# Kernel optimization log

Measured on AMD Instinct MI355X. Metric: run time of the kernel, lower is better.

Reference implementation:

```python
import jax, jax.numpy as jnp
import numpy as np

V, K, H, B = 50000, 50, 300, 512
C_WEIGHTS = 0.0005
C_TOPICS = 5e-06
BN_EPS = 1e-5


def _bn(x, g, b, m, v):
    # eval-mode BatchNorm1d with running stats
    return (x - m) * jax.lax.rsqrt(v + BN_EPS) * g + b


def setup_inputs() -> dict:
    key = jax.random.key(0)
    ks = jax.random.split(key, 16)
    s = 0.02
    inp = {
        "bows": jax.random.uniform(ks[0], (B, V), jnp.float32),
        "normalized_bows": jax.random.uniform(ks[1], (B, V), jnp.float32),
        "labels": jax.random.normal(ks[2], (B,), jnp.float32),
        # encoder q_theta: Linear(V,H) -> relu -> BN -> Linear(H,H) -> relu -> BN
        "W1": jax.random.normal(ks[3], (H, V), jnp.float32) * s,
        "b1": jnp.zeros((H,), jnp.float32),
        "W2": jax.random.normal(ks[4], (H, H), jnp.float32) * s,
        "b2": jnp.zeros((H,), jnp.float32),
        "bn1_g": jnp.ones((H,), jnp.float32),
        "bn1_b": jnp.zeros((H,), jnp.float32),
        "bn1_m": jnp.zeros((H,), jnp.float32),
        "bn1_v": jnp.ones((H,), jnp.float32),
        "bn2_g": jnp.ones((H,), jnp.float32),
        "bn2_b": jnp.zeros((H,), jnp.float32),
        "bn2_m": jnp.zeros((H,), jnp.float32),
        "bn2_v": jnp.ones((H,), jnp.float32),
        "muW": jax.random.normal(ks[5], (K, H), jnp.float32) * s,
        "mub": jnp.zeros((K,), jnp.float32),
        "lsW": jax.random.normal(ks[6], (K, H), jnp.float32) * s,
        "lsb": jnp.zeros((K,), jnp.float32),
        "logit_betas": jax.random.normal(ks[7], (V, K), jnp.float32),
        "gammas": jax.random.normal(ks[8], (V, K), jnp.float32),
        "base_rates": jax.random.normal(ks[9], (V,), jnp.float32),
        "bow_w": jax.random.normal(ks[10], (V,), jnp.float32) * s,
        "bow_b": jnp.zeros((), jnp.float32),
        "topic_w": jax.random.normal(ks[11], (K,), jnp.float32) * s,
        "topic_b": jnp.zeros((), jnp.float32),
    }
    return inp


def reference(bows, normalized_bows, labels, W1, b1, W2, b2,
              bn1_g, bn1_b, bn1_m, bn1_v, bn2_g, bn2_b, bn2_m, bn2_v,
              muW, mub, lsW, lsb, logit_betas, gammas, base_rates,
              bow_w, bow_b, topic_w, topic_b):
    # ---- encode (eval mode: reparameterize returns mu) ----
    h = _bn(jax.nn.relu(normalized_bows @ W1.T + b1), bn1_g, bn1_b, bn1_m, bn1_v)
    h = _bn(jax.nn.relu(h @ W2.T + b2), bn2_g, bn2_b, bn2_m, bn2_v)
    mu = h @ muW.T + mub                       # [B, K]
    logsigma = h @ lsW.T + lsb                 # [B, K]
    kld_theta = -0.5 * jnp.mean(jnp.sum(1.0 + logsigma - mu ** 2 - jnp.exp(logsigma), axis=-1))
    theta = jax.nn.softmax(mu, axis=-1)        # [B, K]

    # ---- decode + reconstruction loss ----
    logits = theta @ logit_betas.T + base_rates          # [B, V]
    preds = jnp.log(jax.nn.softmax(logits, axis=-1) + 1e-06)
    recon_loss = -jnp.mean(jnp.sum(preds * bows, axis=1))

    # ---- other_loss: L1 on base_rates ----
    other_loss = C_WEIGHTS * jnp.sum(jnp.abs(base_rates))

    # ---- predict_labels (hstm-all), reordered contraction: (bows @ scaled_beta) * theta
    scaled_beta = logit_betas * gammas                   # [V, K]
    het_term = jnp.sum((normalized_bows @ scaled_beta) * theta, axis=1)  # == (bows * (theta @ scaled_beta.T)).sum(1)
    expected_pred = het_term + (normalized_bows @ bow_w + bow_b) + (theta @ topic_w + topic_b)

    other_loss = other_loss + jnp.mean((expected_pred - labels) ** 2)
    other_loss = other_loss + C_TOPICS * jnp.sum(jnp.abs(gammas))
    other_loss = other_loss + C_WEIGHTS * jnp.linalg.norm(bow_w)

    return recon_loss, other_loss, kld_theta
```

## Files before the change

kernel.cpp:

```cpp
#include <hip/hip_runtime.h>
#include <hip/hip_bf16.h>
#include <math.h>


#define B_  512
#define V_  50000
#define VP  50016
#define K_  50
#define H_  300
#define KP  64
#define NW  384
#define NSTEP 1563
#define NCVT 7327
#define NSB  782

typedef __attribute__((ext_vector_type(8))) short short8;
typedef __attribute__((ext_vector_type(4))) float f32x4;

static __device__ __forceinline__ short bf16s(float f) {
  unsigned int u = __builtin_bit_cast(unsigned int, f);
  u += 0x7fffu + ((u >> 16) & 1u);
  return (short)(u >> 16);
}

static __device__ __forceinline__ unsigned int pkbf(float lo, float hi) {
  __hip_bfloat162 t = __float22bfloat162_rn(float2{lo, hi});
  unsigned int u; __builtin_memcpy(&u, &t, 4); return u;
}

static __device__ __forceinline__ short8 to_bf8(float4 a, float4 b) {
  unsigned int u[4];
  u[0] = pkbf(a.x, a.y); u[1] = pkbf(a.z, a.w);
  u[2] = pkbf(b.x, b.y); u[3] = pkbf(b.z, b.w);
  short8 r; __builtin_memcpy(&r, u, 16); return r;
}

__global__ __launch_bounds__(256) void k_prep(
    const float* __restrict__ W1,
    const float* __restrict__ beta, const float* __restrict__ gamma,
    const float* __restrict__ br,   const float* __restrict__ bw,
    short* __restrict__ Wcat, short* __restrict__ betab,
    float* __restrict__ pg, float* __restrict__ pbr, float* __restrict__ pbw2)
{
  __shared__ short sbt[64 * 52];
  __shared__ short bbt[64 * 52];
  __shared__ float redA[4];
  const int tid = threadIdx.x;

  if (blockIdx.x < NCVT) {
    const int idx = blockIdx.x * 256 + tid;
    if (idx >= 300 * (VP / 8)) return;
    const int r = idx / (VP / 8);
    const int c = (idx - r * (VP / 8)) * 8;
    short8 outv;
    if (c + 8 <= V_) {
      const float4* p = (const float4*)(W1 + (size_t)r * V_ + c);
      outv = to_bf8(p[0], p[1]);
    } else {
      outv = short8{0, 0, 0, 0, 0, 0, 0, 0};
    }
    *(short8*)(Wcat + (size_t)r * VP + c) = outv;
    return;
  }

  const int blk = blockIdx.x - NCVT;
  const int v0 = blk * 64;
  const int nvalid = (V_ - v0 < 64) ? (V_ - v0) : 64;
  const int nwrite = (VP - v0 < 64) ? (VP - v0) : 64;

  const int nf4 = (nvalid * 50) / 4;
  const float4* bsrc = (const float4*)(beta  + (size_t)v0 * 50);
  const float4* gsrc = (const float4*)(gamma + (size_t)v0 * 50);
  float gabs = 0.f;
  for (int f = tid; f < nf4; f += 256) {
    float4 bv = bsrc[f];
    float4 gv = gsrc[f];
    float be[4] = {bv.x, bv.y, bv.z, bv.w};
    float ge[4] = {gv.x, gv.y, gv.z, gv.w};
    #pragma unroll
    for (int e = 0; e < 4; ++e) {
      int idx = f * 4 + e;
      int j = idx / 50, k = idx - j * 50;
      gabs += fabsf(ge[e]);
      bbt[j * 52 + k] = bf16s(be[e]);
      sbt[j * 52 + k] = bf16s(be[e] * ge[e]);
    }
  }
  #pragma unroll
  for (int off = 1; off < 64; off <<= 1) gabs += __shfl_xor(gabs, off, 64);
  if ((tid & 63) == 0) redA[tid >> 6] = gabs;
  if (tid < 64) {
    float s1 = 0.f, s2 = 0.f;
    if (tid < nvalid) {
      s1 = fabsf(br[v0 + tid]);
      float w = bw[v0 + tid]; s2 = w * w;
    }
    #pragma unroll
    for (int off = 1; off < 64; off <<= 1) {
      s1 += __shfl_xor(s1, off, 64);
      s2 += __shfl_xor(s2, off, 64);
    }
    if (tid == 0) { pbr[blk] = s1; pbw2[blk] = s2; }
  }
  __syncthreads();
  if (tid == 0) pg[blk] = redA[0] + redA[1] + redA[2] + redA[3];

  const int j = tid & 63;
  const int q = tid >> 6;
  #pragma unroll
  for (int p = 0; p < 21; ++p) {
    const int kk = p * 4 + q;
    if (j < nwrite) {
      short val = 0;
      if (j < nvalid) {
        if (kk >= 20 && kk < 70)      val = sbt[j * 52 + (kk - 20)];
        else if (kk == 70)            val = bf16s(bw[v0 + j]);
      }
      Wcat[(size_t)(300 + kk) * VP + v0 + j] = val;
    }
  }
  if (j < nvalid) {
    __attribute__((aligned(16))) short tmp[16];
    #pragma unroll
    for (int t = 0; t < 16; ++t) {
      int k = q * 16 + t;
      tmp[t] = (k < K_) ? bbt[j * 52 + k] : (short)0;
    }
    short8* dst = (short8*)(betab + (size_t)(v0 + j) * 64 + q * 16);
    dst[0] = *(const short8*)&tmp[0];
    dst[1] = *(const short8*)&tmp[8];
  }
}

__global__ __launch_bounds__(256, 2) void k_bg(
    const float* __restrict__ A, const short* __restrict__ Wcat,
    float* __restrict__ part, int sps)
{
  const int t = blockIdx.x;
  const int s = t / 12;
  const int r = t % 12;
  const int bni = r % 3, bmi = r / 3;
  const int lane = threadIdx.x & 63, wv = threadIdx.x >> 6;
  const int l15 = lane & 15, quad = lane >> 4;
  const int m0 = bmi * 128 + (wv & 1) * 64;
  const int n0 = bni * 128 + (wv >> 1) * 64;
  int st0 = s * sps;
  int st1 = st0 + sps; if (st1 > NSTEP) st1 = NSTEP;

  const float* ap[4]; const short* bp[4];
  #pragma unroll
  for (int i = 0; i < 4; ++i) ap[i] = A + (size_t)(m0 + 16 * i + l15) * V_;
  #pragma unroll
  for (int jj = 0; jj < 4; ++jj) bp[jj] = Wcat + (size_t)(n0 + 16 * jj + l15) * VP;

  f32x4 acc[4][4];
  #pragma unroll
  for (int i = 0; i < 4; ++i)
    #pragma unroll
    for (int jj = 0; jj < 4; ++jj) acc[i][jj] = f32x4{0.f, 0.f, 0.f, 0.f};

  float4 A0[4][2], A1[4][2];
  short8 B0[4], B1[4];

  auto ld = [&](int st, float4 (&Ar)[4][2], short8 (&Br)[4]) {
    const int kk = st * 32 + quad * 8;
    if (st != 1562) {
      #pragma unroll
      for (int i = 0; i < 4; ++i) {
        const float4* p = (const float4*)(ap[i] + kk);
        Ar[i][0] = p[0]; Ar[i][1] = p[1];
      }
    } else {
      const float4 z{0.f, 0.f, 0.f, 0.f};
      #pragma unroll
      for (int i = 0; i < 4; ++i) {
        if (quad < 2) {
          const float4* p = (const float4*)(ap[i] + kk);
          Ar[i][0] = p[0]; Ar[i][1] = p[1];
        } else { Ar[i][0] = z; Ar[i][1] = z; }
      }
    }
    #pragma unroll
    for (int jj = 0; jj < 4; ++jj) Br[jj] = *(const short8*)(bp[jj] + kk);
  };
  auto comp = [&](float4 (&Ar)[4][2], short8 (&Br)[4]) {
    short8 af[4];
    #pragma unroll
    for (int i = 0; i < 4; ++i) af[i] = to_bf8(Ar[i][0], Ar[i][1]);
    #pragma unroll
    for (int i = 0; i < 4; ++i)
      #pragma unroll
      for (int jj = 0; jj < 4; ++jj)
        acc[i][jj] = __builtin_amdgcn_mfma_f32_16x16x32_bf16(af[i], Br[jj], acc[i][jj], 0, 0, 0);
  };

  if (st0 < st1) {
    ld(st0, A0, B0);
    int st = st0;
    for (; st + 2 <= st1; st += 2) {
      ld(st + 1, A1, B1);
      comp(A0, B0);
      if (st + 2 < st1) ld(st + 2, A0, B0);
      comp(A1, B1);
    }
    if (st < st1) comp(A0, B0);
  }
  float* op = part + (size_t)s * (B_ * NW);
  #pragma unroll
  for (int i = 0; i < 4; ++i)
    #pragma unroll
    for (int jj = 0; jj < 4; ++jj)
      #pragma unroll
      for (int rr = 0; rr < 4; ++rr)
        op[(size_t)(m0 + 16 * i + quad * 4 + rr) * NW + (n0 + 16 * jj + l15)] = acc[i][jj][rr];
}

__global__ __launch_bounds__(320) void k_mlp(
    const float* __restrict__ part, int S,
    const float* __restrict__ b1,
    const float* __restrict__ g1, const float* __restrict__ bb1,
    const float* __restrict__ m1, const float* __restrict__ v1,
    const float* __restrict__ W2, const float* __restrict__ b2,
    const float* __restrict__ g2, const float* __restrict__ bb2,
    const float* __restrict__ m2, const float* __restrict__ v2,
    const float* __restrict__ muW, const float* __restrict__ mub,
    const float* __restrict__ lsW, const float* __restrict__ lsb,
    short* __restrict__ thetab, float* __restrict__ thetaf,
    float* __restrict__ hetmat, float* __restrict__ kldp)
{
  __shared__ __attribute__((aligned(16))) float h1s[H_];
  __shared__ __attribute__((aligned(16))) float h2s[H_];
  const int b = blockIdx.x;
  const int tid = threadIdx.x;
  const float* pb = part + (size_t)b * NW;

  if (tid < H_) {
    float s0 = 0.f, s1 = 0.f, s2 = 0.f, s3 = 0.f;
    int i = 0;
    for (; i + 4 <= S; i += 4) {
      s0 += pb[(size_t)(i + 0) * (B_ * NW) + tid];
      s1 += pb[(size_t)(i + 1) * (B_ * NW) + tid];
      s2 += pb[(size_t)(i + 2) * (B_ * NW) + tid];
      s3 += pb[(size_t)(i + 3) * (B_ * NW) + tid];
    }
    for (; i < S; ++i) s0 += pb[(size_t)i * (B_ * NW) + tid];
    float s = (s0 + s1) + (s2 + s3);
    float x = fmaxf(s + b1[tid], 0.f);
    h1s[tid] = (x - m1[tid]) * rsqrtf(v1[tid] + 1e-5f) * g1[tid] + bb1[tid];
  }
  if (tid < 51) {
    float s0 = 0.f, s1 = 0.f;
    int i = 0;
    for (; i + 2 <= S; i += 2) {
      s0 += pb[(size_t)(i + 0) * (B_ * NW) + 320 + tid];
      s1 += pb[(size_t)(i + 1) * (B_ * NW) + 320 + tid];
    }
    for (; i < S; ++i) s0 += pb[(size_t)i * (B_ * NW) + 320 + tid];
    hetmat[(size_t)b * KP + tid] = s0 + s1;
  }
  __syncthreads();
  if (tid < H_) {
    const float4* wr = (const float4*)(W2 + (size_t)tid * H_);
    const float4* hr = (const float4*)h1s;
    float acc = 0.f;
    for (int q = 0; q < H_ / 4; ++q) {
      float4 w = wr[q], h = hr[q];
      acc += w.x * h.x + w.y * h.y + w.z * h.z + w.w * h.w;
    }
    float x = fmaxf(acc + b2[tid], 0.f);
    h2s[tid] = (x - m2[tid]) * rsqrtf(v2[tid] + 1e-5f) * g2[tid] + bb2[tid];
  }
  __syncthreads();
  if (tid < 64) {
    float mu = 0.f, ls = 0.f;
    if (tid < K_) {
      const float4* mr = (const float4*)(muW + (size_t)tid * H_);
      const float4* lr = (const float4*)(lsW + (size_t)tid * H_);
      const float4* hr = (const float4*)h2s;
      for (int q = 0; q < H_ / 4; ++q) {
        float4 h = hr[q], a = mr[q], c = lr[q];
        mu += a.x * h.x + a.y * h.y + a.z * h.z + a.w * h.w;
        ls += c.x * h.x + c.y * h.y + c.z * h.z + c.w * h.w;
      }
      mu += mub[tid]; ls += lsb[tid];
    }
    float term = (tid < K_) ? (1.f + ls - mu * mu - __expf(ls)) : 0.f;
    float ts = term;
    #pragma unroll
    for (int off = 1; off < 64; off <<= 1) ts += __shfl_xor(ts, off, 64);
    if (tid == 0) kldp[b] = ts;
    float mv = (tid < K_) ? mu : -INFINITY;
    #pragma unroll
    for (int off = 1; off < 64; off <<= 1) mv = fmaxf(mv, __shfl_xor(mv, off, 64));
    float e = (tid < K_) ? __expf(mu - mv) : 0.f;
    float se = e;
    #pragma unroll
    for (int off = 1; off < 64; off <<= 1) se += __shfl_xor(se, off, 64);
    float tv = (tid < K_) ? (e / se) : 0.f;
    thetaf[(size_t)b * KP + tid] = tv;
    thetab[(size_t)b * KP + tid] = bf16s(tv);
  }
}

__global__ __launch_bounds__(256, 2) void k_c1(
    const short* __restrict__ thetab, const short* __restrict__ betab,
    const float* __restrict__ br, float* __restrict__ c1p)
{
  const int blk = blockIdx.x;
  const int bm = blk & 7, vs = blk >> 3;
  const int lane = threadIdx.x & 63, wv = threadIdx.x >> 6;
  const int l15 = lane & 15, quad = lane >> 4;
  const int b0 = bm * 64 + wv * 16;
  const short8* arow = (const short8*)(thetab + (size_t)(b0 + l15) * KP);
  const short8 a0 = arow[quad], a1 = arow[4 + quad];
  int t0 = vs * 33, t1 = t0 + 33; if (t1 > 3125) t1 = 3125;
  float p0 = 0.f, p1 = 0.f, p2 = 0.f, p3 = 0.f;
  auto body = [&](int tt) {
    const int v0 = tt * 16;
    const short8* brow = (const short8*)(betab + (size_t)(v0 + l15) * KP);
    short8 q0 = brow[quad], q1 = brow[4 + quad];
    f32x4 acc = {0.f, 0.f, 0.f, 0.f};
    acc = __builtin_amdgcn_mfma_f32_16x16x32_bf16(a0, q0, acc, 0, 0, 0);
    acc = __builtin_amdgcn_mfma_f32_16x16x32_bf16(a1, q1, acc, 0, 0, 0);
    const float brv = br[v0 + l15];
    p0 += __expf(acc[0] + brv);
    p1 += __expf(acc[1] + brv);
    p2 += __expf(acc[2] + brv);
    p3 += __expf(acc[3] + brv);
  };
  int tt = t0;
  for (; tt + 2 <= t1; tt += 2) { body(tt); body(tt + 1); }
  if (tt < t1) body(tt);
  #pragma unroll
  for (int off = 1; off < 16; off <<= 1) {
    p0 += __shfl_xor(p0, off, 16);
    p1 += __shfl_xor(p1, off, 16);
    p2 += __shfl_xor(p2, off, 16);
    p3 += __shfl_xor(p3, off, 16);
  }
  if (l15 == 0) {
    float* dst = c1p + (size_t)vs * B_ + b0 + quad * 4;
    dst[0] = p0; dst[1] = p1; dst[2] = p2; dst[3] = p3;
  }
}

static __device__ __forceinline__ float blockred512(float x, float* red) {
  #pragma unroll
  for (int off = 1; off < 64; off <<= 1) x += __shfl_xor(x, off, 64);
  if ((threadIdx.x & 63) == 0) red[threadIdx.x >> 6] = x;
  __syncthreads();
  float r = 0.f;
  if (threadIdx.x == 0)
    for (int i = 0; i < 8; ++i) r += red[i];
  __syncthreads();
  return r;
}

__global__ __launch_bounds__(512) void k_d1(
    const float* __restrict__ c1p, const float* __restrict__ kldp,
    const float* __restrict__ pg, const float* __restrict__ pbr,
    const float* __restrict__ pbw2,
    const float* __restrict__ hetmat, const float* __restrict__ thetaf,
    const float* __restrict__ labels, const float* __restrict__ topic_w,
    const float* __restrict__ topic_b, const float* __restrict__ bow_b,
    float* __restrict__ lseb, float* __restrict__ out)
{
  __shared__ float red[8];
  const int b = threadIdx.x;
  float se = 0.f;
  for (int i = 0; i < 96; ++i) se += c1p[(size_t)i * B_ + b];
  lseb[b] = __logf(se);
  float het = 0.f, tpc = 0.f;
  #pragma unroll
  for (int k = 0; k < K_; ++k) {
    float th = thetaf[(size_t)b * KP + k];
    het += th * hetmat[(size_t)b * KP + k];
    tpc += th * topic_w[k];
  }
  float ep = het + hetmat[(size_t)b * KP + 50] + bow_b[0] + tpc + topic_b[0];
  float d = ep - labels[b];
  float mse  = blockred512(d * d, red);
  float kl   = blockred512(kldp[b], red);
  float sg = 0.f, sr = 0.f, sw = 0.f;
  for (int i = b; i < NSB; i += 512) { sg += pg[i]; sr += pbr[i]; sw += pbw2[i]; }
  sg = blockred512(sg, red);
  sr = blockred512(sr, red);
  sw = blockred512(sw, red);
  if (b == 0) {
    out[1] = 0.0005f * sr + mse / (float)B_ + 5e-6f * sg + 0.0005f * sqrtf(sw);
    out[2] = -0.5f * kl / (float)B_;
  }
}

__global__ __launch_bounds__(256, 2) void k_c2(
    const short* __restrict__ thetab, const short* __restrict__ betab,
    const float* __restrict__ br, const float* __restrict__ lseb,
    const float* __restrict__ bows, float* __restrict__ c2p)
{
  __shared__ float red[4];
  const int blk = blockIdx.x;
  const int bm = blk & 7, vs = blk >> 3;
  const int lane = threadIdx.x & 63, wv = threadIdx.x >> 6;
  const int l15 = lane & 15, quad = lane >> 4;
  const int b0 = bm * 64 + wv * 16;
  const short8* arow = (const short8*)(thetab + (size_t)(b0 + l15) * KP);
  const short8 a0 = arow[quad], a1 = arow[4 + quad];
  float lse4[4]; const float* bro[4];
  #pragma unroll
  for (int rr = 0; rr < 4; ++rr) {
    lse4[rr] = lseb[b0 + quad * 4 + rr];
    bro[rr] = bows + (size_t)(b0 + quad * 4 + rr) * V_;
  }
  int t0 = vs * 33, t1 = t0 + 33; if (t1 > 3125) t1 = 3125;
  float p = 0.f;
  auto body = [&](int tt) {
    const int v0 = tt * 16;
    const int v = v0 + l15;
    const short8* brow = (const short8*)(betab + (size_t)v * KP);
    short8 q0 = brow[quad], q1 = brow[4 + quad];
    f32x4 acc = {0.f, 0.f, 0.f, 0.f};
    acc = __builtin_amdgcn_mfma_f32_16x16x32_bf16(a0, q0, acc, 0, 0, 0);
    acc = __builtin_amdgcn_mfma_f32_16x16x32_bf16(a1, q1, acc, 0, 0, 0);
    const float brv = br[v];
    #pragma unroll
    for (int rr = 0; rr < 4; ++rr) {
      float l = acc[rr] + brv - lse4[rr];
      float pr = __logf(__expf(l) + 1e-6f);
      p += pr * bro[rr][v];
    }
  };
  int tt = t0;
  for (; tt + 2 <= t1; tt += 2) { body(tt); body(tt + 1); }
  if (tt < t1) body(tt);
  #pragma unroll
  for (int off = 1; off < 64; off <<= 1) p += __shfl_xor(p, off, 64);
  if (lane == 0) red[wv] = p;
  __syncthreads();
  if (threadIdx.x == 0) c2p[blk] = red[0] + red[1] + red[2] + red[3];
}

__global__ __launch_bounds__(256) void k_d2(
    const float* __restrict__ c2p, float* __restrict__ out)
{
  __shared__ float red[4];
  float s = 0.f;
  for (int i = threadIdx.x; i < 768; i += 256) s += c2p[i];
  #pragma unroll
  for (int off = 1; off < 64; off <<= 1) s += __shfl_xor(s, off, 64);
  if ((threadIdx.x & 63) == 0) red[threadIdx.x >> 6] = s;
  __syncthreads();
  if (threadIdx.x == 0)
    out[0] = -(red[0] + red[1] + red[2] + red[3]) / (float)B_;
}

extern "C" void kernel_launch(void* const* d_in, const int* in_sizes, int n_in,
                              void* d_out, int out_size, void* d_ws, size_t ws_size,
                              hipStream_t stream)
{
  const float* bows    = (const float*)d_in[0];
  const float* nb      = (const float*)d_in[1];
  const float* labels  = (const float*)d_in[2];
  const float* W1      = (const float*)d_in[3];
  const float* b1      = (const float*)d_in[4];
  const float* W2      = (const float*)d_in[5];
  const float* b2      = (const float*)d_in[6];
  const float* bn1_g   = (const float*)d_in[7];
  const float* bn1_b   = (const float*)d_in[8];
  const float* bn1_m   = (const float*)d_in[9];
  const float* bn1_v   = (const float*)d_in[10];
  const float* bn2_g   = (const float*)d_in[11];
  const float* bn2_b   = (const float*)d_in[12];
  const float* bn2_m   = (const float*)d_in[13];
  const float* bn2_v   = (const float*)d_in[14];
  const float* muW     = (const float*)d_in[15];
  const float* mub     = (const float*)d_in[16];
  const float* lsW     = (const float*)d_in[17];
  const float* lsb     = (const float*)d_in[18];
  const float* beta    = (const float*)d_in[19];
  const float* gamma   = (const float*)d_in[20];
  const float* brates  = (const float*)d_in[21];
  const float* bow_w   = (const float*)d_in[22];
  const float* bow_b   = (const float*)d_in[23];
  const float* topic_w = (const float*)d_in[24];
  const float* topic_b = (const float*)d_in[25];
  float* out = (float*)d_out;

  char* ws = (char*)d_ws;
  size_t off = 0;
  auto take = [&](size_t bytes) { void* p = ws + off; off = (off + bytes + 255) & ~(size_t)255; return p; };

  short* Wcat    = (short*)take((size_t)NW * VP * 2);
  short* betab   = (short*)take((size_t)V_ * 64 * 2);
  short* thetab  = (short*)take((size_t)B_ * KP * 2);
  float* thetaf  = (float*)take((size_t)B_ * KP * 4);
  float* hetmat  = (float*)take((size_t)B_ * KP * 4);
  float* kldp    = (float*)take((size_t)B_ * 4);
  float* c1p     = (float*)take((size_t)96 * B_ * 4);
  float* c2p     = (float*)take((size_t)768 * 4);
  float* lse_    = (float*)take((size_t)B_ * 4);
  float* pg      = (float*)take((size_t)NSB * 4);
  float* pbr     = (float*)take((size_t)NSB * 4);
  float* pbw2    = (float*)take((size_t)NSB * 4);
  float* part1   = (float*)(ws + off);
  size_t remain = (ws_size > off) ? (ws_size - off) : 0;
  int S = (int)(remain / ((size_t)B_ * NW * 4));
  if (S > 42) S = 42;
  if (S < 1)  S = 1;
  const int sps = (NSTEP + S - 1) / S;

  k_prep<<<NCVT + NSB, 256, 0, stream>>>(W1, beta, gamma, brates, bow_w,
                                         Wcat, betab, pg, pbr, pbw2);
  k_bg  <<<12 * S, 256, 0, stream>>>(nb, Wcat, part1, sps);
  k_mlp <<<B_, 320, 0, stream>>>(part1, S, b1, bn1_g, bn1_b, bn1_m, bn1_v,
                                 W2, b2, bn2_g, bn2_b, bn2_m, bn2_v,
                                 muW, mub, lsW, lsb, thetab, thetaf, hetmat, kldp);
  k_c1  <<<8 * 96, 256, 0, stream>>>(thetab, betab, brates, c1p);
  k_d1  <<<1, 512, 0, stream>>>(c1p, kldp, pg, pbr, pbw2, hetmat, thetaf,
                                labels, topic_w, topic_b, bow_b, lse_, out);
  k_c2  <<<8 * 96, 256, 0, stream>>>(thetab, betab, brates, lse_, bows, c2p);
  k_d2  <<<1, 256, 0, stream>>>(c2p, out);
}
```

Before: 494.5 us.

## Pre-convert activations to bf16 in step-blocked layout for contiguous GEMM loads

The prep kernel now converts normalized_bows to bf16 as well as W1, and writes both into a k-step-blocked layout (32-wide k chunks, rows contiguous per step). The GEMM kernel then loads ready bf16 fragments through simple pointer increments instead of reading fp32 rows and converting them inside the loop. The change also raises occupancy to 3 blocks per SM and the split-K cap from 42 to 64. In exchange there is an extra conversion pass over the 512x50000 activation matrix, adding a bf16 write and read-back of roughly 51 MB, plus more partial sums for the MLP kernel to reduce.

```diff
diff --git a/kernel.cpp b/kernel.cpp
--- a/kernel.cpp
+++ b/kernel.cpp
@@ -13,6 +13,7 @@
 #define NSTEP 1563
 #define NCVT 7327
 #define NSB  782
+#define NACV 12504
 
 typedef __attribute__((ext_vector_type(8))) short short8;
 typedef __attribute__((ext_vector_type(4))) float f32x4;
@@ -39,27 +40,45 @@
     const float* __restrict__ W1,
     const float* __restrict__ beta, const float* __restrict__ gamma,
     const float* __restrict__ br,   const float* __restrict__ bw,
-    short* __restrict__ Wcat, short* __restrict__ betab,
+    const float* __restrict__ nb,
+    short* __restrict__ Wcatb, short* __restrict__ betab,
+    short* __restrict__ nbb,
     float* __restrict__ pg, float* __restrict__ pbr, float* __restrict__ pbw2)
 {
   __shared__ short sbt[64 * 52];
   __shared__ short bbt[64 * 52];
   __shared__ float redA[4];
   const int tid = threadIdx.x;
+  const short8 z8 = {0, 0, 0, 0, 0, 0, 0, 0};
 
   if (blockIdx.x < NCVT) {
     const int idx = blockIdx.x * 256 + tid;
-    if (idx >= 300 * (VP / 8)) return;
-    const int r = idx / (VP / 8);
-    const int c = (idx - r * (VP / 8)) * 8;
-    short8 outv;
-    if (c + 8 <= V_) {
-      const float4* p = (const float4*)(W1 + (size_t)r * V_ + c);
-      outv = to_bf8(p[0], p[1]);
-    } else {
-      outv = short8{0, 0, 0, 0, 0, 0, 0, 0};
-    }
-    *(short8*)(Wcat + (size_t)r * VP + c) = outv;
+    if (idx >= NSTEP * 300 * 4) return;
+    const int st = idx / 1200;
+    const int rem = idx - st * 1200;
+    const int n = rem >> 2, kq = rem & 3;
+    const int kbase = st * 32 + kq * 8;
+    short8 o = z8;
+    if (kbase + 8 <= V_) {
+      const float4* p = (const float4*)(W1 + (size_t)n * V_ + kbase);
+      o = to_bf8(p[0], p[1]);
+    }
+    *(short8*)(Wcatb + (size_t)st * 12288 + n * 32 + kq * 8) = o;
+    return;
+  }
+
+  if (blockIdx.x >= NCVT + NSB) {
+    const int idx = (blockIdx.x - (NCVT + NSB)) * 256 + tid;
+    const int st = idx >> 11;
+    const int r  = (idx >> 2) & 511;
+    const int kq = idx & 3;
+    const int kbase = st * 32 + kq * 8;
+    short8 o = z8;
+    if (kbase + 8 <= V_) {
+      const float4* p = (const float4*)(nb + (size_t)r * V_ + kbase);
+      o = to_bf8(p[0], p[1]);
+    }
+    *(short8*)(nbb + (size_t)st * 16384 + r * 32 + kq * 8) = o;
     return;
   }
 
@@ -116,7 +135,7 @@
         if (kk >= 20 && kk < 70)      val = sbt[j * 52 + (kk - 20)];
         else if (kk == 70)            val = bf16s(bw[v0 + j]);
       }
-      Wcat[(size_t)(300 + kk) * VP + v0 + j] = val;
+      Wcatb[(size_t)(blk * 2 + (j >> 5)) * 12288 + (300 + kk) * 32 + (j & 31)] = val;
     }
   }
   if (j < nvalid) {
@@ -132,8 +151,8 @@
   }
 }
 
-__global__ __launch_bounds__(256, 2) void k_bg(
-    const float* __restrict__ A, const short* __restrict__ Wcat,
+__global__ __launch_bounds__(256, 3) void k_bg(
+    const short* __restrict__ Ab, const short* __restrict__ Bb,
     float* __restrict__ part, int sps)
 {
   const int t = blockIdx.x;
@@ -144,14 +163,13 @@
   const int l15 = lane & 15, quad = lane >> 4;
   const int m0 = bmi * 128 + (wv & 1) * 64;
   const int n0 = bni * 128 + (wv >> 1) * 64;
-  int st0 = s * sps;
-  int st1 = st0 + sps; if (st1 > NSTEP) st1 = NSTEP;
-
-  const float* ap[4]; const short* bp[4];
-  #pragma unroll
-  for (int i = 0; i < 4; ++i) ap[i] = A + (size_t)(m0 + 16 * i + l15) * V_;
-  #pragma unroll
-  for (int jj = 0; jj < 4; ++jj) bp[jj] = Wcat + (size_t)(n0 + 16 * jj + l15) * VP;
+  int st0 = s * sps, st1 = st0 + sps;
+  if (st0 > NSTEP) st0 = NSTEP;
+  if (st1 > NSTEP) st1 = NSTEP;
+  const int nst = st1 - st0;
+
+  const short8* pa = (const short8*)Ab + (size_t)st0 * 2048 + (m0 + l15) * 4 + quad;
+  const short8* pb = (const short8*)Bb + (size_t)st0 * 1536 + (n0 + l15) * 4 + quad;
 
   f32x4 acc[4][4];
   #pragma unroll
@@ -159,52 +177,35 @@
     #pragma unroll
     for (int jj = 0; jj < 4; ++jj) acc[i][jj] = f32x4{0.f, 0.f, 0.f, 0.f};
 
-  float4 A0[4][2], A1[4][2];
-  short8 B0[4], B1[4];
-
-  auto ld = [&](int st, float4 (&Ar)[4][2], short8 (&Br)[4]) {
-    const int kk = st * 32 + quad * 8;
-    if (st != 1562) {
-      #pragma unroll
-      for (int i = 0; i < 4; ++i) {
-        const float4* p = (const float4*)(ap[i] + kk);
-        Ar[i][0] = p[0]; Ar[i][1] = p[1];
-      }
-    } else {
-      const float4 z{0.f, 0.f, 0.f, 0.f};
-      #pragma unroll
-      for (int i = 0; i < 4; ++i) {
-        if (quad < 2) {
-          const float4* p = (const float4*)(ap[i] + kk);
-          Ar[i][0] = p[0]; Ar[i][1] = p[1];
-        } else { Ar[i][0] = z; Ar[i][1] = z; }
-      }
-    }
-    #pragma unroll
-    for (int jj = 0; jj < 4; ++jj) Br[jj] = *(const short8*)(bp[jj] + kk);
+  short8 A0[4], A1[4], B0[4], B1[4];
+
+  auto ld = [&](short8 (&Af)[4], short8 (&Bf)[4]) {
+    #pragma unroll
+    for (int i = 0; i < 4; ++i) Af[i] = pa[i * 64];
+    #pragma unroll
+    for (int jj = 0; jj < 4; ++jj) Bf[jj] = pb[jj * 64];
+    pa += 2048; pb += 1536;
   };
-  auto comp = [&](float4 (&Ar)[4][2], short8 (&Br)[4]) {
-    short8 af[4];
-    #pragma unroll
-    for (int i = 0; i < 4; ++i) af[i] = to_bf8(Ar[i][0], Ar[i][1]);
+  auto comp = [&](short8 (&Af)[4], short8 (&Bf)[4]) {
     #pragma unroll
     for (int i = 0; i < 4; ++i)
       #pragma unroll
       for (int jj = 0; jj < 4; ++jj)
-        acc[i][jj] = __builtin_amdgcn_mfma_f32_16x16x32_bf16(af[i], Br[jj], acc[i][jj], 0, 0, 0);
+        acc[i][jj] = __builtin_amdgcn_mfma_f32_16x16x32_bf16(Af[i], Bf[jj], acc[i][jj], 0, 0, 0);
   };
 
-  if (st0 < st1) {
-    ld(st0, A0, B0);
-    int st = st0;
-    for (; st + 2 <= st1; st += 2) {
-      ld(st + 1, A1, B1);
+  if (nst > 0) {
+    ld(A0, B0);
+    int k = 0;
+    for (; k + 2 <= nst; k += 2) {
+      ld(A1, B1);
       comp(A0, B0);
-      if (st + 2 < st1) ld(st + 2, A0, B0);
+      if (k + 2 < nst) ld(A0, B0);
       comp(A1, B1);
     }
-    if (st < st1) comp(A0, B0);
-  }
+    if (k < nst) comp(A0, B0);
+  }
+
   float* op = part + (size_t)s * (B_ * NW);
   #pragma unroll
   for (int i = 0; i < 4; ++i)
@@ -489,7 +490,8 @@
   size_t off = 0;
   auto take = [&](size_t bytes) { void* p = ws + off; off = (off + bytes + 255) & ~(size_t)255; return p; };
 
-  short* Wcat    = (short*)take((size_t)NW * VP * 2);
+  short* Wcatb   = (short*)take((size_t)NSTEP * 12288 * 2);
+  short* nbb     = (short*)take((size_t)NSTEP * 16384 * 2);
   short* betab   = (short*)take((size_t)V_ * 64 * 2);
   short* thetab  = (short*)take((size_t)B_ * KP * 2);
   float* thetaf  = (float*)take((size_t)B_ * KP * 4);
@@ -504,13 +506,13 @@
   float* part1   = (float*)(ws + off);
   size_t remain = (ws_size > off) ? (ws_size - off) : 0;
   int S = (int)(remain / ((size_t)B_ * NW * 4));
-  if (S > 42) S = 42;
+  if (S > 64) S = 64;
   if (S < 1)  S = 1;
   const int sps = (NSTEP + S - 1) / S;
 
-  k_prep<<<NCVT + NSB, 256, 0, stream>>>(W1, beta, gamma, brates, bow_w,
-                                         Wcat, betab, pg, pbr, pbw2);
-  k_bg  <<<12 * S, 256, 0, stream>>>(nb, Wcat, part1, sps);
+  k_prep<<<NCVT + NSB + NACV, 256, 0, stream>>>(
+      W1, beta, gamma, brates, bow_w, nb, Wcatb, betab, nbb, pg, pbr, pbw2);
+  k_bg  <<<12 * S, 256, 0, stream>>>(nbb, Wcatb, part1, sps);
   k_mlp <<<B_, 320, 0, stream>>>(part1, S, b1, bn1_g, bn1_b, bn1_m, bn1_v,
                                  W2, b2, bn2_g, bn2_b, bn2_m, bn2_v,
                                  muW, mub, lsW, lsb, thetab, thetaf, hetmat, kldp);
```

Measured after the change: 479.2 us. 1.03x faster.
